# Kernel tuning notes

Measured on AMD Instinct MI355X. Metric: run time of the kernel, lower is better.

Reference implementation:

```python
import jax, jax.numpy as jnp
import numpy as np
from jax import lax

KERNEL_SIZE = 11
SIGMA = 1.5
C1 = 0.01 ** 2
C2 = 0.03 ** 2


def _gaussian_kernel(channels):
    x = np.arange(KERNEL_SIZE, dtype=np.float32) - (KERNEL_SIZE // 2)
    g = np.exp(-(x ** 2) / (2.0 * SIGMA ** 2))
    g = g / g.sum()
    k2 = np.outer(g, g).astype(np.float32)  # (k, k)
    # depthwise weight layout OIHW with I=1, O=channels
    return jnp.asarray(np.broadcast_to(k2, (channels, 1, KERNEL_SIZE, KERNEL_SIZE)))


def _blur(x, kernel):
    # depthwise gaussian conv, SAME padding (padding = k//2, odd kernel, stride 1)
    return lax.conv_general_dilated(
        x, kernel,
        window_strides=(1, 1),
        padding='SAME',
        dimension_numbers=('NCHW', 'OIHW', 'NCHW'),
        feature_group_count=x.shape[1],
    )


def setup_inputs() -> dict:
    key = jax.random.key(0)
    k1, k2 = jax.random.split(key)
    img1 = jax.random.uniform(k1, (16, 3, 512, 512), dtype=jnp.float32)
    img2 = jax.random.uniform(k2, (16, 3, 512, 512), dtype=jnp.float32)
    return {"img1": img1, "img2": img2}


def reference(img1, img2):
    kernel = _gaussian_kernel(img1.shape[1]).astype(img1.dtype)
    mu1 = _blur(img1, kernel)
    mu2 = _blur(img2, kernel)
    mu1_sq = mu1 * mu1
    mu2_sq = mu2 * mu2
    mu1_mu2 = mu1 * mu2
    sigma1_sq = _blur(img1 * img1, kernel) - mu1_sq
    sigma2_sq = _blur(img2 * img2, kernel) - mu2_sq
    sigma12 = _blur(img1 * img2, kernel) - mu1_mu2
    ssim_map = ((2 * mu1_mu2 + C1) * (2 * sigma12 + C2)) / (
        (mu1_sq + mu2_sq + C1) * (sigma1_sq + sigma2_sq + C2))
    return jnp.mean(ssim_map)
```

## Files before the change

kernel.cpp:

```cpp
#include <hip/hip_runtime.h>
#include <math.h>

#define WIDTH   512
#define NPLANE  48
#define TILE    32
#define HALO    5
#define NROWS   42
#define SSTR    52
#define HBS     48
#define GRIDX   16
#define NBLOCKS (GRIDX*GRIDX*NPLANE)
#define NPIX    (16.0*3.0*512.0*512.0)

struct GaussW { float w[11]; };

union SU {
    float s[2][NROWS][SSTR];
    float hb[5 * 32 * HBS];
};

__device__ __forceinline__ void blur16(const float* vin, const GaussW& gw, float* o)
{
    #pragma unroll
    for (int t = 0; t < 16; ++t) {
        float s = vin[t] * gw.w[0];
        #pragma unroll
        for (int k = 1; k < 11; ++k) s = fmaf(gw.w[k], vin[t + k], s);
        o[t] = s;
    }
}

__global__ __launch_bounds__(256, 4)
void ssim_tile_kernel(const float* __restrict__ img1,
                      const float* __restrict__ img2,
                      float* __restrict__ partial, GaussW gw)
{
    __shared__ __align__(16) SU su;
    __shared__ float red[4];

    const int tid = threadIdx.x;
    const int bx = blockIdx.x, by = blockIdx.y, bz = blockIdx.z;
    const float* __restrict__ p1 = img1 + (size_t)bz * (WIDTH * WIDTH);
    const float* __restrict__ p2 = img2 + (size_t)bz * (WIDTH * WIDTH);
    const int gx0 = bx * TILE - 8;
    const int gy0 = by * TILE - HALO;

    const bool interior = ((unsigned)(bx - 1) < 14u) & ((unsigned)(by - 1) < 14u);

    if (interior) {
        #pragma unroll
        for (int k = 0; k < 4; ++k) {
            int l = tid + (k << 8);
            if (l < 1008) {
                int img = l >= 504;
                int u2  = img ? l - 504 : l;
                int r   = u2 / 12;
                int p   = u2 - r * 12;
                const float* gp = (img ? p2 : p1) + (gy0 + r) * WIDTH + (gx0 + (p << 2));
                *(float4*)&su.s[img][r][p << 2] = *(const float4*)gp;
            }
        }
    } else {
        #pragma unroll
        for (int k = 0; k < 4; ++k) {
            int l = tid + (k << 8);
            if (l < 1008) {
                int img = l >= 504;
                int u2  = img ? l - 504 : l;
                int r   = u2 / 12;
                int p   = u2 - r * 12;
                int gr = gy0 + r, gc = gx0 + (p << 2);
                float4 v = make_float4(0.f, 0.f, 0.f, 0.f);
                if ((unsigned)gr < WIDTH && (unsigned)gc <= (WIDTH - 4))
                    v = *(const float4*)((img ? p2 : p1) + gr * WIDTH + gc);
                *(float4*)&su.s[img][r][p << 2] = v;
            }
        }
    }
    __syncthreads();

    const bool active = tid < 252;
    float oa[16], ob[16];
    int qa = 0, qb = 0, r = 0, c0 = 0, g = 0;
    if (active) {
        g = (tid >= 84) + (tid >= 168);
        int u2 = tid - g * 84;
        r  = u2 >> 1;
        c0 = (u2 & 1) << 4;
        float ld[32];
        if (g < 2) {
            const float* sp = &su.s[g][r][c0];
            #pragma unroll
            for (int p = 0; p < 8; ++p) {
                float4 v = *(const float4*)(sp + (p << 2));
                ld[4*p] = v.x; ld[4*p+1] = v.y; ld[4*p+2] = v.z; ld[4*p+3] = v.w;
            }
            blur16(ld + 3, gw, oa);
            #pragma unroll
            for (int i = 0; i < 26; ++i) ld[3 + i] *= ld[3 + i];
            blur16(ld + 3, gw, ob);
            qa = g; qb = g + 2;
        } else {
            float lb[32];
            const float* spa = &su.s[0][r][c0];
            const float* spb = &su.s[1][r][c0];
            #pragma unroll
            for (int p = 0; p < 8; ++p) {
                float4 v = *(const float4*)(spa + (p << 2));
                ld[4*p] = v.x; ld[4*p+1] = v.y; ld[4*p+2] = v.z; ld[4*p+3] = v.w;
                float4 w2 = *(const float4*)(spb + (p << 2));
                lb[4*p] = w2.x; lb[4*p+1] = w2.y; lb[4*p+2] = w2.z; lb[4*p+3] = w2.w;
            }
            #pragma unroll
            for (int i = 0; i < 26; ++i) ld[3 + i] *= lb[3 + i];
            blur16(ld + 3, gw, oa);
            qa = 4;
        }
    }
    __syncthreads();

    if (active) {
        int ba = (qa * 32 + c0) * HBS;
        #pragma unroll
        for (int j = 0; j < 16; ++j)
            su.hb[ba + j * HBS + (r ^ ((j & 3) << 2))] = oa[j];
        if (g < 2) {
            int bb = (qb * 32 + c0) * HBS;
            #pragma unroll
            for (int j = 0; j < 16; ++j)
                su.hb[bb + j * HBS + (r ^ ((j & 3) << 2))] = ob[j];
        }
    }
    __syncthreads();

    const int c   = tid & 31;
    const int r0  = (tid >> 5) << 2;
    const int swz = (c & 3) << 2;
    float acc[5][4];
    #pragma unroll
    for (int q = 0; q < 5; ++q) {
        const int base = (q * 32 + c) * HBS;
        float win[16];
        #pragma unroll
        for (int k = 0; k < 4; ++k) {
            int rr = (r0 + (k << 2)) ^ swz;
            float4 v = *(const float4*)&su.hb[base + rr];
            win[4*k] = v.x; win[4*k+1] = v.y; win[4*k+2] = v.z; win[4*k+3] = v.w;
        }
        #pragma unroll
        for (int i = 0; i < 4; ++i) {
            float s = win[i] * gw.w[0];
            #pragma unroll
            for (int k = 1; k < 11; ++k) s = fmaf(gw.w[k], win[i + k], s);
            acc[q][i] = s;
        }
    }

    const float C1 = 0.01f * 0.01f, C2 = 0.03f * 0.03f;
    float ssum = 0.f;
    #pragma unroll
    for (int i = 0; i < 4; ++i) {
        float a = acc[0][i], b = acc[1][i];
        float ab = a * b, a2 = a * a, b2 = b * b;
        float s11 = acc[2][i] - a2;
        float s22 = acc[3][i] - b2;
        float s12 = acc[4][i] - ab;
        float num = (2.f * ab + C1) * (2.f * s12 + C2);
        float den = (a2 + b2 + C1) * (s11 + s22 + C2);
        ssum += num / den;
    }

    #pragma unroll
    for (int off = 32; off > 0; off >>= 1) ssum += __shfl_down(ssum, off);
    if ((tid & 63) == 0) red[tid >> 6] = ssum;
    __syncthreads();
    if (tid == 0)
        partial[bx + GRIDX * (by + GRIDX * bz)] = red[0] + red[1] + red[2] + red[3];
}

__global__ __launch_bounds__(1024)
void ssim_reduce_kernel(const float* __restrict__ partial, float* __restrict__ out)
{
    __shared__ double red[16];
    double s = 0.0;
    for (int i = threadIdx.x; i < NBLOCKS; i += 1024) s += (double)partial[i];
    #pragma unroll
    for (int off = 32; off > 0; off >>= 1) s += __shfl_down(s, off);
    if ((threadIdx.x & 63) == 0) red[threadIdx.x >> 6] = s;
    __syncthreads();
    if (threadIdx.x == 0) {
        double t = 0.0;
        #pragma unroll
        for (int w = 0; w < 16; ++w) t += red[w];
        out[0] = (float)(t / NPIX);
    }
}

extern "C" void kernel_launch(void* const* d_in, const int* in_sizes, int n_in,
                              void* d_out, int out_size, void* d_ws, size_t ws_size,
                              hipStream_t stream)
{
    GaussW gw;
    double g[11], sum = 0.0;
    for (int i = 0; i < 11; ++i) {
        double x = (double)(i - 5);
        g[i] = exp(-(x * x) / 4.5);
        sum += g[i];
    }
    for (int i = 0; i < 11; ++i) gw.w[i] = (float)(g[i] / sum);

    const float* img1 = (const float*)d_in[0];
    const float* img2 = (const float*)d_in[1];
    float* partial = (float*)d_ws;
    float* out = (float*)d_out;

    dim3 grid(GRIDX, GRIDX, NPLANE);
    hipLaunchKernelGGL(ssim_tile_kernel, grid, dim3(256), 0, stream,
                       img1, img2, partial, gw);
    hipLaunchKernelGGL(ssim_reduce_kernel, dim3(1), dim3(1024), 0, stream,
                       partial, out);
}
```

Before: 186.0 us.

## Fuse final reduction into tile kernel via last-block atomic counter and rotate LDS swizzle

Drops the separate single-block reduce kernel. Each tile block now stores its partial sum and atomically bumps a global counter, and the last block to finish reduces all partials in double precision. This removes one kernel launch and its dependency gap, but adds a memset of the counter each call. The LDS swizzle for the horizontal-blur buffer also changes from an XOR pattern to a modular rotation by (col&7)*4, meant to spread bank accesses across more banks during the transposed writes and float4 reads.

```diff
diff --git a/kernel.cpp b/kernel.cpp
--- a/kernel.cpp
+++ b/kernel.cpp
@@ -33,10 +33,13 @@
 __global__ __launch_bounds__(256, 4)
 void ssim_tile_kernel(const float* __restrict__ img1,
                       const float* __restrict__ img2,
-                      float* __restrict__ partial, GaussW gw)
+                      float* __restrict__ partial,
+                      unsigned int* __restrict__ counter,
+                      float* __restrict__ out, GaussW gw)
 {
     __shared__ __align__(16) SU su;
     __shared__ float red[4];
+    __shared__ int isLast;
 
     const int tid = threadIdx.x;
     const int bx = blockIdx.x, by = blockIdx.y, bz = blockIdx.z;
@@ -120,22 +123,28 @@
     __syncthreads();
 
     if (active) {
-        int ba = (qa * 32 + c0) * HBS;
-        #pragma unroll
-        for (int j = 0; j < 16; ++j)
-            su.hb[ba + j * HBS + (r ^ ((j & 3) << 2))] = oa[j];
+        #pragma unroll
+        for (int j = 0; j < 16; ++j) {
+            int col  = c0 + j;
+            int slot = r + ((col & 7) << 2);
+            if (slot >= HBS) slot -= HBS;
+            su.hb[(qa * 32 + col) * HBS + slot] = oa[j];
+        }
         if (g < 2) {
-            int bb = (qb * 32 + c0) * HBS;
-            #pragma unroll
-            for (int j = 0; j < 16; ++j)
-                su.hb[bb + j * HBS + (r ^ ((j & 3) << 2))] = ob[j];
-        }
-    }
-    __syncthreads();
-
-    const int c   = tid & 31;
-    const int r0  = (tid >> 5) << 2;
-    const int swz = (c & 3) << 2;
+            #pragma unroll
+            for (int j = 0; j < 16; ++j) {
+                int col  = c0 + j;
+                int slot = r + ((col & 7) << 2);
+                if (slot >= HBS) slot -= HBS;
+                su.hb[(qb * 32 + col) * HBS + slot] = ob[j];
+            }
+        }
+    }
+    __syncthreads();
+
+    const int c  = tid & 31;
+    const int r0 = (tid >> 5) << 2;
+    const int R  = (c & 7) << 2;
     float acc[5][4];
     #pragma unroll
     for (int q = 0; q < 5; ++q) {
@@ -143,8 +152,9 @@
         float win[16];
         #pragma unroll
         for (int k = 0; k < 4; ++k) {
-            int rr = (r0 + (k << 2)) ^ swz;
-            float4 v = *(const float4*)&su.hb[base + rr];
+            int s0 = r0 + (k << 2) + R;
+            if (s0 >= HBS) s0 -= HBS;
+            float4 v = *(const float4*)&su.hb[base + s0];
             win[4*k] = v.x; win[4*k+1] = v.y; win[4*k+2] = v.z; win[4*k+3] = v.w;
         }
         #pragma unroll
@@ -174,25 +184,30 @@
     for (int off = 32; off > 0; off >>= 1) ssum += __shfl_down(ssum, off);
     if ((tid & 63) == 0) red[tid >> 6] = ssum;
     __syncthreads();
-    if (tid == 0)
-        partial[bx + GRIDX * (by + GRIDX * bz)] = red[0] + red[1] + red[2] + red[3];
-}
-
-__global__ __launch_bounds__(1024)
-void ssim_reduce_kernel(const float* __restrict__ partial, float* __restrict__ out)
-{
-    __shared__ double red[16];
-    double s = 0.0;
-    for (int i = threadIdx.x; i < NBLOCKS; i += 1024) s += (double)partial[i];
-    #pragma unroll
-    for (int off = 32; off > 0; off >>= 1) s += __shfl_down(s, off);
-    if ((threadIdx.x & 63) == 0) red[threadIdx.x >> 6] = s;
-    __syncthreads();
-    if (threadIdx.x == 0) {
-        double t = 0.0;
-        #pragma unroll
-        for (int w = 0; w < 16; ++w) t += red[w];
-        out[0] = (float)(t / NPIX);
+
+    if (tid == 0) {
+        int bid = bx + GRIDX * (by + GRIDX * bz);
+        float bsum = red[0] + red[1] + red[2] + red[3];
+        __hip_atomic_store(&partial[bid], bsum, __ATOMIC_RELAXED,
+                           __HIP_MEMORY_SCOPE_AGENT);
+        unsigned int old = __hip_atomic_fetch_add(counter, 1u, __ATOMIC_ACQ_REL,
+                                                  __HIP_MEMORY_SCOPE_AGENT);
+        isLast = (old == (unsigned)(NBLOCKS - 1));
+    }
+    __syncthreads();
+
+    if (isLast) {
+        double s = 0.0;
+        for (int i = tid; i < NBLOCKS; i += 256)
+            s += (double)__hip_atomic_load(&partial[i], __ATOMIC_RELAXED,
+                                           __HIP_MEMORY_SCOPE_AGENT);
+        #pragma unroll
+        for (int off = 32; off > 0; off >>= 1) s += __shfl_down(s, off);
+        __shared__ double dred[4];
+        if ((tid & 63) == 0) dred[tid >> 6] = s;
+        __syncthreads();
+        if (tid == 0)
+            out[0] = (float)((dred[0] + dred[1] + dred[2] + dred[3]) / NPIX);
     }
 }
 
@@ -211,12 +226,13 @@
 
     const float* img1 = (const float*)d_in[0];
     const float* img2 = (const float*)d_in[1];
-    float* partial = (float*)d_ws;
+    unsigned int* counter = (unsigned int*)d_ws;
+    float* partial = (float*)((char*)d_ws + 16);
     float* out = (float*)d_out;
+
+    hipMemsetAsync(d_ws, 0, 16, stream);
 
     dim3 grid(GRIDX, GRIDX, NPLANE);
     hipLaunchKernelGGL(ssim_tile_kernel, grid, dim3(256), 0, stream,
-                       img1, img2, partial, gw);
-    hipLaunchKernelGGL(ssim_reduce_kernel, dim3(1), dim3(1024), 0, stream,
-                       partial, out);
+                       img1, img2, partial, counter, out, gw);
 }
```

Measured after the change: 422.5 us. 2.27x slower.
